# Kernel tuning notes

Measured on AMD Instinct MI355X. Metric: run time of the kernel, lower is better.

Reference implementation:

```python
import jax, jax.numpy as jnp
import numpy as np

EMBED_DIM = 256
NUM_HEADS = 8
WINDOW = 64
HEAD_DIM = EMBED_DIM // NUM_HEADS


def setup_inputs() -> dict:
    key = jax.random.key(0)
    k_x, k_w, k_ow = jax.random.split(key, 3)
    B, S, E = 2, 4096, EMBED_DIM
    x = jax.random.normal(k_x, (B, S, E), dtype=jnp.float32)
    # nn.MultiheadAttention params: packed in_proj (q,k,v) and out_proj
    bound = 1.0 / np.sqrt(E)
    in_proj_w = jax.random.uniform(k_w, (3 * E, E), jnp.float32, -bound, bound)
    in_proj_b = jnp.zeros((3 * E,), jnp.float32)
    out_w = jax.random.uniform(k_ow, (E, E), jnp.float32, -bound, bound)
    out_b = jnp.zeros((E,), jnp.float32)
    return {"x": x, "in_proj_w": in_proj_w, "in_proj_b": in_proj_b,
            "out_w": out_w, "out_b": out_b}


def reference(x, in_proj_w, in_proj_b, out_w, out_b):
    B, S, E = x.shape
    H, D = NUM_HEADS, HEAD_DIM
    # packed qkv projection (torch Linear: y = x @ W^T + b)
    qkv = jnp.einsum('bse,fe->bsf', x, in_proj_w) + in_proj_b  # [B,S,3E]
    q, k, v = jnp.split(qkv, 3, axis=-1)
    q = q.reshape(B, S, H, D).transpose(0, 2, 1, 3)  # [B,H,S,D]
    k = k.reshape(B, S, H, D).transpose(0, 2, 1, 3)
    v = v.reshape(B, S, H, D).transpose(0, 2, 1, 3)
    scale = 1.0 / jnp.sqrt(jnp.asarray(D, x.dtype))
    scores = jnp.einsum('bhqd,bhkd->bhqk', q * scale, k)  # [B,H,S,S]
    idx = jnp.arange(S)
    band = jnp.abs(idx[:, None] - idx[None, :]) <= WINDOW  # [S,S]
    neg = jnp.asarray(-1e9, scores.dtype)
    scores = jnp.where(band[None, None, :, :], scores, neg)
    attn = jax.nn.softmax(scores, axis=-1)
    out = jnp.einsum('bhqk,bhkd->bhqd', attn, v)  # [B,H,S,D]
    out = out.transpose(0, 2, 1, 3).reshape(B, S, E)
    return jnp.einsum('bse,fe->bsf', out, out_w) + out_b
```

## Files before the change

### kernel.cpp

```cpp
#include <hip/hip_runtime.h>
#include <hip/hip_bf16.h>

#define S_LEN 4096
#define EMB   256
#define NHEAD 8
#define HDIM  32
#define WIN   64
#define BATCH 2

typedef __attribute__((ext_vector_type(8))) short short8;
typedef __attribute__((ext_vector_type(4))) float floatx4;
typedef unsigned short u16;
typedef unsigned int   u32;

static __device__ __forceinline__ u32 bf16_rn(float x) {
    u32 u = __float_as_uint(x);
    return (u + 0x7FFFu + ((u >> 16) & 1u)) >> 16;
}
static __device__ __forceinline__ u32 packsplit(float x) {
    const u32 hi = bf16_rn(x);
    const float hf = __uint_as_float(hi << 16);
    const u32 lo = bf16_rn(x - hf);
    return (hi << 16) | lo;
}
static __device__ __forceinline__ void unpack_pair(u32 p0, u32 p1, u32& h, u32& l) {
    h = (p0 >> 16) | (p1 & 0xFFFF0000u);
    l = (p0 & 0xFFFFu) | (p1 << 16);
}
static __device__ __forceinline__ void unpack8(uint4 a, uint4 b, uint4& h, uint4& l) {
    unpack_pair(a.x, a.y, h.x, l.x);
    unpack_pair(a.z, a.w, h.y, l.y);
    unpack_pair(b.x, b.y, h.z, l.z);
    unpack_pair(b.z, b.w, h.w, l.w);
}

#define NX4 524288
#define NW4 49152
#define NO4 16384

__global__ __launch_bounds__(256) void convert_kernel(
    const float* __restrict__ X, const float* __restrict__ Wi, const float* __restrict__ Wo,
    u32* __restrict__ Xp, u32* __restrict__ Wip, u32* __restrict__ Wop)
{
    const int i = blockIdx.x * 256 + threadIdx.x;
    const float* src; u32* dst; int off;
    if (i < NX4)            { src = X;  dst = Xp;  off = i; }
    else if (i < NX4 + NW4) { src = Wi; dst = Wip; off = i - NX4; }
    else                    { src = Wo; dst = Wop; off = i - NX4 - NW4; }
    const float4 v = *(const float4*)(src + (size_t)off * 4);
    uint4 o;
    o.x = packsplit(v.x); o.y = packsplit(v.y);
    o.z = packsplit(v.z); o.w = packsplit(v.w);
    *(uint4*)(dst + (size_t)off * 4) = o;
}

#define LDA 40

__global__ __launch_bounds__(256) void qkv_proj_kernel(
    const u32* __restrict__ Xp, const u32* __restrict__ Wp,
    const float* __restrict__ bias,
    u32* __restrict__ Qp, u32* __restrict__ Kp, u32* __restrict__ Vp)
{
    __shared__ __align__(16) u16 Ah[128 * LDA], Al[128 * LDA];
    __shared__ __align__(16) u16 Bh[64 * LDA],  Bl[64 * LDA];
    const int tid = threadIdx.x;
    const int m0 = blockIdx.y * 128, n0 = blockIdx.x * 64;
    const int srow = tid >> 2, sc = tid & 3;
    const int lane = tid & 63, wv = tid >> 6;
    const int wm = (wv >> 1) * 64, wn = (wv & 1) * 32;
    const int lm = lane & 15, kq = lane >> 4;

    uint4 pA[2][2], pB[2];
#pragma unroll
    for (int r = 0; r < 2; ++r) {
        const u32* base = Xp + (size_t)(m0 + srow + r * 64) * EMB + sc * 8;
        pA[r][0] = *(const uint4*)base;
        pA[r][1] = *(const uint4*)(base + 4);
    }
    {
        const u32* base = Wp + (size_t)(n0 + srow) * EMB + sc * 8;
        pB[0] = *(const uint4*)base;
        pB[1] = *(const uint4*)(base + 4);
    }

    floatx4 acc[4][2] = {};
    for (int t = 0; t < 8; ++t) {
        __syncthreads();
#pragma unroll
        for (int r = 0; r < 2; ++r) {
            uint4 h, l;
            unpack8(pA[r][0], pA[r][1], h, l);
            *(uint4*)&Ah[(srow + r * 64) * LDA + sc * 8] = h;
            *(uint4*)&Al[(srow + r * 64) * LDA + sc * 8] = l;
        }
        {
            uint4 h, l;
            unpack8(pB[0], pB[1], h, l);
            *(uint4*)&Bh[srow * LDA + sc * 8] = h;
            *(uint4*)&Bl[srow * LDA + sc * 8] = l;
        }
        __syncthreads();
        if (t < 7) {
            const int k0 = (t + 1) * 32;
#pragma unroll
            for (int r = 0; r < 2; ++r) {
                const u32* base = Xp + (size_t)(m0 + srow + r * 64) * EMB + k0 + sc * 8;
                pA[r][0] = *(const uint4*)base;
                pA[r][1] = *(const uint4*)(base + 4);
            }
            const u32* base = Wp + (size_t)(n0 + srow) * EMB + k0 + sc * 8;
            pB[0] = *(const uint4*)base;
            pB[1] = *(const uint4*)(base + 4);
        }
        short8 a_h[4], a_l[4], b_h[2], b_l[2];
#pragma unroll
        for (int mt = 0; mt < 4; ++mt) {
            a_h[mt] = *(const short8*)&Ah[(wm + mt * 16 + lm) * LDA + kq * 8];
            a_l[mt] = *(const short8*)&Al[(wm + mt * 16 + lm) * LDA + kq * 8];
        }
#pragma unroll
        for (int nt = 0; nt < 2; ++nt) {
            b_h[nt] = *(const short8*)&Bh[(wn + nt * 16 + lm) * LDA + kq * 8];
            b_l[nt] = *(const short8*)&Bl[(wn + nt * 16 + lm) * LDA + kq * 8];
        }
#pragma unroll
        for (int mt = 0; mt < 4; ++mt)
#pragma unroll
            for (int nt = 0; nt < 2; ++nt) {
                acc[mt][nt] = __builtin_amdgcn_mfma_f32_16x16x32_bf16(a_h[mt], b_h[nt], acc[mt][nt], 0, 0, 0);
                acc[mt][nt] = __builtin_amdgcn_mfma_f32_16x16x32_bf16(a_h[mt], b_l[nt], acc[mt][nt], 0, 0, 0);
                acc[mt][nt] = __builtin_amdgcn_mfma_f32_16x16x32_bf16(a_l[mt], b_h[nt], acc[mt][nt], 0, 0, 0);
            }
    }
#pragma unroll
    for (int nt = 0; nt < 2; ++nt) {
        const int f = n0 + wn + nt * 16 + lm;
        const int which = f >> 8;
        const int h = (f & 255) >> 5, d = f & 31;
        u32* dst = (which == 0) ? Qp : ((which == 1) ? Kp : Vp);
        const float sc2 = (which == 0) ? 0.17677669529663687f : 1.0f;
        const float bf = bias[f];
#pragma unroll
        for (int mt = 0; mt < 4; ++mt)
#pragma unroll
            for (int r = 0; r < 4; ++r) {
                const int m = m0 + wm + mt * 16 + kq * 4 + r;
                const int b = m >> 12, s = m & (S_LEN - 1);
                dst[(((size_t)b * NHEAD + h) * S_LEN + s) * HDIM + d]
                    = packsplit((acc[mt][nt][r] + bf) * sc2);
            }
    }
}

__global__ __launch_bounds__(256) void out_proj_kernel(
    const u32* __restrict__ Abp, const u32* __restrict__ Wp,
    const float* __restrict__ bias, float* __restrict__ C)
{
    __shared__ __align__(16) u16 Ah[64 * LDA], Al[64 * LDA];
    __shared__ __align__(16) u16 Bh[64 * LDA], Bl[64 * LDA];
    const int tid = threadIdx.x;
    const int m0 = blockIdx.y * 64, n0 = blockIdx.x * 64;
    const int srow = tid >> 2, sc = tid & 3;
    const int lane = tid & 63, wv = tid >> 6;
    const int wm = (wv >> 1) * 32, wn = (wv & 1) * 32;
    const int lm = lane & 15, kq = lane >> 4;

    uint4 pA[2], pB[2];
    {
        const u32* base = Abp + (size_t)(m0 + srow) * EMB + sc * 8;
        pA[0] = *(const uint4*)base;
        pA[1] = *(const uint4*)(base + 4);
    }
    {
        const u32* base = Wp + (size_t)(n0 + srow) * EMB + sc * 8;
        pB[0] = *(const uint4*)base;
        pB[1] = *(const uint4*)(base + 4);
    }

    floatx4 acc[2][2] = {};
    for (int t = 0; t < 8; ++t) {
        __syncthreads();
        {
            uint4 h, l;
            unpack8(pA[0], pA[1], h, l);
            *(uint4*)&Ah[srow * LDA + sc * 8] = h;
            *(uint4*)&Al[srow * LDA + sc * 8] = l;
        }
        {
            uint4 h, l;
            unpack8(pB[0], pB[1], h, l);
            *(uint4*)&Bh[srow * LDA + sc * 8] = h;
            *(uint4*)&Bl[srow * LDA + sc * 8] = l;
        }
        __syncthreads();
        if (t < 7) {
            const int k0 = (t + 1) * 32;
            {
                const u32* base = Abp + (size_t)(m0 + srow) * EMB + k0 + sc * 8;
                pA[0] = *(const uint4*)base;
                pA[1] = *(const uint4*)(base + 4);
            }
            const u32* base = Wp + (size_t)(n0 + srow) * EMB + k0 + sc * 8;
            pB[0] = *(const uint4*)base;
            pB[1] = *(const uint4*)(base + 4);
        }
        short8 a_h[2], a_l[2], b_h[2], b_l[2];
#pragma unroll
        for (int mt = 0; mt < 2; ++mt) {
            a_h[mt] = *(const short8*)&Ah[(wm + mt * 16 + lm) * LDA + kq * 8];
            a_l[mt] = *(const short8*)&Al[(wm + mt * 16 + lm) * LDA + kq * 8];
        }
#pragma unroll
        for (int nt = 0; nt < 2; ++nt) {
            b_h[nt] = *(const short8*)&Bh[(wn + nt * 16 + lm) * LDA + kq * 8];
            b_l[nt] = *(const short8*)&Bl[(wn + nt * 16 + lm) * LDA + kq * 8];
        }
#pragma unroll
        for (int mt = 0; mt < 2; ++mt)
#pragma unroll
            for (int nt = 0; nt < 2; ++nt) {
                acc[mt][nt] = __builtin_amdgcn_mfma_f32_16x16x32_bf16(a_h[mt], b_h[nt], acc[mt][nt], 0, 0, 0);
                acc[mt][nt] = __builtin_amdgcn_mfma_f32_16x16x32_bf16(a_h[mt], b_l[nt], acc[mt][nt], 0, 0, 0);
                acc[mt][nt] = __builtin_amdgcn_mfma_f32_16x16x32_bf16(a_l[mt], b_h[nt], acc[mt][nt], 0, 0, 0);
            }
    }
#pragma unroll
    for (int nt = 0; nt < 2; ++nt) {
        const int f = n0 + wn + nt * 16 + lm;
        const float bf = bias[f];
#pragma unroll
        for (int mt = 0; mt < 2; ++mt)
#pragma unroll
            for (int r = 0; r < 4; ++r) {
                const int m = m0 + wm + mt * 16 + kq * 4 + r;
                C[(size_t)m * EMB + f] = acc[mt][nt][r] + bf;
            }
    }
}

#define AKS 40
#define AVS 200

__global__ __launch_bounds__(256) void local_attn_kernel(
    const u32* __restrict__ Qp, const u32* __restrict__ Kp,
    const u32* __restrict__ Vp, u32* __restrict__ Abp)
{
    __shared__ __align__(16) u16 Kh[192 * AKS], Kl[192 * AKS];
    __shared__ __align__(16) u16 Vt[32 * AVS];

    const int tid = threadIdx.x;
    const int q0 = blockIdx.x * 64;
    const int h = blockIdx.y, b = blockIdx.z;
    const int jmin = max(0, q0 - WIN);
    const int jmax = min(S_LEN - 1, q0 + 63 + WIN);
    const int nk = jmax - jmin + 1;
    const size_t bhS = ((size_t)b * NHEAD + h) * S_LEN;
    const size_t qoff = (bhS + q0) * HDIM;
    const size_t koff = (bhS + jmin) * HDIM;

    const int lane = tid & 63, wv = tid >> 6;
    const int lm = lane & 15, quad = lane >> 4;
    const int qbase = wv * 16;

    const u32* qb = Qp + qoff + (size_t)(qbase + lm) * HDIM + quad * 8;
    const uint4 qp0 = *(const uint4*)qb;
    const uint4 qp1 = *(const uint4*)(qb + 4);

    const int srow = tid >> 2, sc = tid & 3;
#pragma unroll
    for (int r = 0; r < 3; ++r) {
        const int t = srow + r * 64;
        const int tc = min(t, nk - 1);
        const u32* base = Kp + koff + (size_t)tc * HDIM + sc * 8;
        uint4 h4, l4;
        unpack8(*(const uint4*)base, *(const uint4*)(base + 4), h4, l4);
        *(uint4*)&Kh[t * AKS + sc * 8] = h4;
        *(uint4*)&Kl[t * AKS + sc * 8] = l4;
    }
#pragma unroll
    for (int r = 0; r < 3; ++r) {
        const int t = srow + r * 64;
        const int tc = min(t, nk - 1);
        const u32* base = Vp + koff + (size_t)tc * HDIM + sc * 8;
        const uint4 v0 = *(const uint4*)base;
        const uint4 v1 = *(const uint4*)(base + 4);
        const int d0 = sc * 8;
        Vt[(d0 + 0) * AVS + t] = (u16)(v0.x >> 16);
        Vt[(d0 + 1) * AVS + t] = (u16)(v0.y >> 16);
        Vt[(d0 + 2) * AVS + t] = (u16)(v0.z >> 16);
        Vt[(d0 + 3) * AVS + t] = (u16)(v0.w >> 16);
        Vt[(d0 + 4) * AVS + t] = (u16)(v1.x >> 16);
        Vt[(d0 + 5) * AVS + t] = (u16)(v1.y >> 16);
        Vt[(d0 + 6) * AVS + t] = (u16)(v1.z >> 16);
        Vt[(d0 + 7) * AVS + t] = (u16)(v1.w >> 16);
    }

    short8 qh, ql;
    {
        uint4 h4, l4;
        unpack8(qp0, qp1, h4, l4);
        qh = *(const short8*)&h4;
        ql = *(const short8*)&l4;
    }

    __syncthreads();

    const int tb = max(0, ((wv >> 1) << 1) + (min(q0 - WIN, 0) >> 4));

    floatx4 sacc[10];
#pragma unroll
    for (int i = 0; i < 10; ++i) {
        const int nt = tb + i;
        const short8 kh = *(const short8*)&Kh[(nt * 16 + lm) * AKS + quad * 8];
        const short8 kl = *(const short8*)&Kl[(nt * 16 + lm) * AKS + quad * 8];
        floatx4 a = {};
        a = __builtin_amdgcn_mfma_f32_16x16x32_bf16(kh, qh, a, 0, 0, 0);
        a = __builtin_amdgcn_mfma_f32_16x16x32_bf16(kh, ql, a, 0, 0, 0);
        a = __builtin_amdgcn_mfma_f32_16x16x32_bf16(kl, qh, a, 0, 0, 0);
        sacc[i] = a;
    }

    const int qr = q0 + qbase + lm;
    float mx = -1e30f;
#pragma unroll
    for (int i = 0; i < 10; ++i) {
        const int sbase = (tb + i) * 16 + quad * 4;
#pragma unroll
        for (int r = 0; r < 4; ++r) {
            const int slot = sbase + r;
            const int keyg = jmin + slot;
            const bool valid = (slot < nk) && (keyg >= qr - WIN) && (keyg <= qr + WIN);
            const float sv = valid ? sacc[i][r] : -1e30f;
            sacc[i][r] = sv;
            mx = fmaxf(mx, sv);
        }
    }
    mx = fmaxf(mx, __shfl_xor(mx, 16));
    mx = fmaxf(mx, __shfl_xor(mx, 32));

    float l = 0.f;
    u32 pk_[20];
#pragma unroll
    for (int i = 0; i < 10; ++i) {
        const float p0 = __expf(sacc[i][0] - mx);
        const float p1 = __expf(sacc[i][1] - mx);
        const float p2 = __expf(sacc[i][2] - mx);
        const float p3 = __expf(sacc[i][3] - mx);
        l += (p0 + p1) + (p2 + p3);
        pk_[2 * i]     = bf16_rn(p0) | (bf16_rn(p1) << 16);
        pk_[2 * i + 1] = bf16_rn(p2) | (bf16_rn(p3) << 16);
    }
    l += __shfl_xor(l, 16);
    l += __shfl_xor(l, 32);
    const float rl = 1.f / l;

    const int kb = tb >> 1;
    floatx4 oacc[2] = {};
#pragma unroll
    for (int i = 0; i < 5; ++i) {
        const int ks = kb + i;
        uint4 aw;
        aw.x = pk_[4 * i + 0];
        aw.y = pk_[4 * i + 1];
        aw.z = pk_[4 * i + 2];
        aw.w = pk_[4 * i + 3];
        const short8 ap = *(const short8*)&aw;
        const int sb = ks * 32 + quad * 4;
        const uint2 e0 = *(const uint2*)&Vt[lm * AVS + sb];
        const uint2 o0 = *(const uint2*)&Vt[lm * AVS + sb + 16];
        const uint2 e1 = *(const uint2*)&Vt[(16 + lm) * AVS + sb];
        const uint2 o1 = *(const uint2*)&Vt[(16 + lm) * AVS + sb + 16];
        uint4 bw0; bw0.x = e0.x; bw0.y = e0.y; bw0.z = o0.x; bw0.w = o0.y;
        uint4 bw1; bw1.x = e1.x; bw1.y = e1.y; bw1.z = o1.x; bw1.w = o1.y;
        const short8 bv0 = *(const short8*)&bw0;
        const short8 bv1 = *(const short8*)&bw1;
        oacc[0] = __builtin_amdgcn_mfma_f32_16x16x32_bf16(ap, bv0, oacc[0], 0, 0, 0);
        oacc[1] = __builtin_amdgcn_mfma_f32_16x16x32_bf16(ap, bv1, oacc[1], 0, 0, 0);
    }

    float rlr[4];
#pragma unroll
    for (int r = 0; r < 4; ++r) rlr[r] = __shfl(rl, quad * 4 + r);
#pragma unroll
    for (int nt = 0; nt < 2; ++nt)
#pragma unroll
        for (int r = 0; r < 4; ++r) {
            const int qrow = qbase + quad * 4 + r;
            Abp[((size_t)b * S_LEN + q0 + qrow) * EMB + h * HDIM + nt * 16 + lm]
                = packsplit(oacc[nt][r] * rlr[r]);
        }
}

extern "C" void kernel_launch(void* const* d_in, const int* in_sizes, int n_in,
                              void* d_out, int out_size, void* d_ws, size_t ws_size,
                              hipStream_t stream) {
    const float* x  = (const float*)d_in[0];
    const float* wi = (const float*)d_in[1];
    const float* bi = (const float*)d_in[2];
    const float* wo = (const float*)d_in[3];
    const float* bo = (const float*)d_in[4];
    float* out = (float*)d_out;

    const size_t per = (size_t)BATCH * NHEAD * S_LEN * HDIM;
    u32* p = (u32*)d_ws;
    u32* Xp  = p; p += per;
    u32* Wip = p; p += 768 * EMB;
    u32* Wop = p; p += EMB * EMB;
    u32* Qp  = p; p += per;
    u32* Kp  = p; p += per;
    u32* Vp  = p; p += per;
    u32* Abp = p; p += per;

    convert_kernel<<<dim3((NX4 + NW4 + NO4) / 256), 256, 0, stream>>>(
        x, wi, wo, Xp, Wip, Wop);
    qkv_proj_kernel<<<dim3(768 / 64, 8192 / 128), 256, 0, stream>>>(
        Xp, Wip, bi, Qp, Kp, Vp);
    local_attn_kernel<<<dim3(S_LEN / 64, NHEAD, BATCH), 256, 0, stream>>>(
        Qp, Kp, Vp, Abp);
    out_proj_kernel<<<dim3(256 / 64, 8192 / 64), 256, 0, stream>>>(
        Abp, Wop, bo, out);
}
```

Baseline: 110.9 us.

## Split hi/lo bf16 planes and stage GEMM tiles via direct global-to-LDS loads

Intermediate tensors are stored as separate hi and lo bf16 planes instead of interleaved packed u32, which removes the unpack shuffles in every consumer. V now keeps only its hi plane, since only that part was ever used. The projection GEMMs load tiles with global_load_lds into double-buffered, XOR-swizzled LDS, and remap the block order for locality. This gives up register prefetching and padded LDS for a direct async copy path with one barrier per k-step. That path depends on swizzle correctness and on whether the hardware honours the 16-byte LDS load.

```diff
diff --git a/kernel.cpp b/kernel.cpp
--- a/kernel.cpp
+++ b/kernel.cpp
@@ -10,6 +10,7 @@
 
 typedef __attribute__((ext_vector_type(8))) short short8;
 typedef __attribute__((ext_vector_type(4))) float floatx4;
+typedef __attribute__((ext_vector_type(4))) unsigned short ushort4v;
 typedef unsigned short u16;
 typedef unsigned int   u32;
 
@@ -17,21 +18,11 @@
     u32 u = __float_as_uint(x);
     return (u + 0x7FFFu + ((u >> 16) & 1u)) >> 16;
 }
-static __device__ __forceinline__ u32 packsplit(float x) {
-    const u32 hi = bf16_rn(x);
-    const float hf = __uint_as_float(hi << 16);
-    const u32 lo = bf16_rn(x - hf);
-    return (hi << 16) | lo;
-}
-static __device__ __forceinline__ void unpack_pair(u32 p0, u32 p1, u32& h, u32& l) {
-    h = (p0 >> 16) | (p1 & 0xFFFF0000u);
-    l = (p0 & 0xFFFFu) | (p1 << 16);
-}
-static __device__ __forceinline__ void unpack8(uint4 a, uint4 b, uint4& h, uint4& l) {
-    unpack_pair(a.x, a.y, h.x, l.x);
-    unpack_pair(a.z, a.w, h.y, l.y);
-    unpack_pair(b.x, b.y, h.z, l.z);
-    unpack_pair(b.z, b.w, h.w, l.w);
+
+static __device__ __forceinline__ void gload16(const u16* g, u16* l) {
+    __builtin_amdgcn_global_load_lds(
+        (const __attribute__((address_space(1))) void*)g,
+        (__attribute__((address_space(3))) void*)l, 16, 0, 0);
 }
 
 #define NX4 524288
@@ -40,88 +31,83 @@
 
 __global__ __launch_bounds__(256) void convert_kernel(
     const float* __restrict__ X, const float* __restrict__ Wi, const float* __restrict__ Wo,
-    u32* __restrict__ Xp, u32* __restrict__ Wip, u32* __restrict__ Wop)
+    u16* __restrict__ Xh, u16* __restrict__ Xl,
+    u16* __restrict__ Wih, u16* __restrict__ Wil,
+    u16* __restrict__ Woh, u16* __restrict__ Wol)
 {
     const int i = blockIdx.x * 256 + threadIdx.x;
-    const float* src; u32* dst; int off;
-    if (i < NX4)            { src = X;  dst = Xp;  off = i; }
-    else if (i < NX4 + NW4) { src = Wi; dst = Wip; off = i - NX4; }
-    else                    { src = Wo; dst = Wop; off = i - NX4 - NW4; }
+    const float* src; u16 *dh, *dl; int off;
+    if (i < NX4)            { src = X;  dh = Xh;  dl = Xl;  off = i; }
+    else if (i < NX4 + NW4) { src = Wi; dh = Wih; dl = Wil; off = i - NX4; }
+    else                    { src = Wo; dh = Woh; dl = Wol; off = i - NX4 - NW4; }
     const float4 v = *(const float4*)(src + (size_t)off * 4);
-    uint4 o;
-    o.x = packsplit(v.x); o.y = packsplit(v.y);
-    o.z = packsplit(v.z); o.w = packsplit(v.w);
-    *(uint4*)(dst + (size_t)off * 4) = o;
-}
-
-#define LDA 40
+    ushort4v h, l;
+    {
+        u32 hb;
+        hb = bf16_rn(v.x); h.x = (u16)hb; l.x = (u16)bf16_rn(v.x - __uint_as_float(hb << 16));
+        hb = bf16_rn(v.y); h.y = (u16)hb; l.y = (u16)bf16_rn(v.y - __uint_as_float(hb << 16));
+        hb = bf16_rn(v.z); h.z = (u16)hb; l.z = (u16)bf16_rn(v.z - __uint_as_float(hb << 16));
+        hb = bf16_rn(v.w); h.w = (u16)hb; l.w = (u16)bf16_rn(v.w - __uint_as_float(hb << 16));
+    }
+    *(ushort4v*)(dh + (size_t)off * 4) = h;
+    *(ushort4v*)(dl + (size_t)off * 4) = l;
+}
+
+#define BK 32
 
 __global__ __launch_bounds__(256) void qkv_proj_kernel(
-    const u32* __restrict__ Xp, const u32* __restrict__ Wp,
+    const u16* __restrict__ Xh, const u16* __restrict__ Xl,
+    const u16* __restrict__ Wh, const u16* __restrict__ Wl,
     const float* __restrict__ bias,
-    u32* __restrict__ Qp, u32* __restrict__ Kp, u32* __restrict__ Vp)
+    u16* __restrict__ Qh, u16* __restrict__ Ql,
+    u16* __restrict__ Kh, u16* __restrict__ Kl,
+    u16* __restrict__ Vh)
 {
-    __shared__ __align__(16) u16 Ah[128 * LDA], Al[128 * LDA];
-    __shared__ __align__(16) u16 Bh[64 * LDA],  Bl[64 * LDA];
+    __shared__ __align__(16) u16 SA[2][2][128 * BK];
+    __shared__ __align__(16) u16 SB[2][2][64 * BK];
+
     const int tid = threadIdx.x;
-    const int m0 = blockIdx.y * 128, n0 = blockIdx.x * 64;
-    const int srow = tid >> 2, sc = tid & 3;
+    const int wg0 = blockIdx.y * 12 + blockIdx.x;
+    const int wg = (wg0 & 7) * 96 + (wg0 >> 3);
+    const int n0 = (wg % 12) * 64, m0 = (wg / 12) * 128;
     const int lane = tid & 63, wv = tid >> 6;
+    const int lm = lane & 15, kq = lane >> 4;
+    const int gr = lane >> 2;
+    const int gc = ((lane & 3) ^ ((lane >> 3) & 3)) * 8;
+    const int swz = (lm >> 1) & 3;
     const int wm = (wv >> 1) * 64, wn = (wv & 1) * 32;
-    const int lm = lane & 15, kq = lane >> 4;
-
-    uint4 pA[2][2], pB[2];
-#pragma unroll
-    for (int r = 0; r < 2; ++r) {
-        const u32* base = Xp + (size_t)(m0 + srow + r * 64) * EMB + sc * 8;
-        pA[r][0] = *(const uint4*)base;
-        pA[r][1] = *(const uint4*)(base + 4);
-    }
-    {
-        const u32* base = Wp + (size_t)(n0 + srow) * EMB + sc * 8;
-        pB[0] = *(const uint4*)base;
-        pB[1] = *(const uint4*)(base + 4);
-    }
+
+    auto stage = [&](int buf, int k0) {
+#pragma unroll
+        for (int cc = 0; cc < 2; ++cc) {
+            const int c = 2 * wv + cc;
+            const size_t grow = (size_t)(m0 + 16 * c + gr) * EMB + k0 + gc;
+            gload16(Xh + grow, &SA[buf][0][c * 512]);
+            gload16(Xl + grow, &SA[buf][1][c * 512]);
+        }
+        const size_t brow = (size_t)(n0 + 16 * wv + gr) * EMB + k0 + gc;
+        gload16(Wh + brow, &SB[buf][0][wv * 512]);
+        gload16(Wl + brow, &SB[buf][1][wv * 512]);
+    };
 
     floatx4 acc[4][2] = {};
+    stage(0, 0);
+    __syncthreads();
+    int cur = 0;
     for (int t = 0; t < 8; ++t) {
-        __syncthreads();
-#pragma unroll
-        for (int r = 0; r < 2; ++r) {
-            uint4 h, l;
-            unpack8(pA[r][0], pA[r][1], h, l);
-            *(uint4*)&Ah[(srow + r * 64) * LDA + sc * 8] = h;
-            *(uint4*)&Al[(srow + r * 64) * LDA + sc * 8] = l;
-        }
-        {
-            uint4 h, l;
-            unpack8(pB[0], pB[1], h, l);
-            *(uint4*)&Bh[srow * LDA + sc * 8] = h;
-            *(uint4*)&Bl[srow * LDA + sc * 8] = l;
-        }
-        __syncthreads();
-        if (t < 7) {
-            const int k0 = (t + 1) * 32;
-#pragma unroll
-            for (int r = 0; r < 2; ++r) {
-                const u32* base = Xp + (size_t)(m0 + srow + r * 64) * EMB + k0 + sc * 8;
-                pA[r][0] = *(const uint4*)base;
-                pA[r][1] = *(const uint4*)(base + 4);
-            }
-            const u32* base = Wp + (size_t)(n0 + srow) * EMB + k0 + sc * 8;
-            pB[0] = *(const uint4*)base;
-            pB[1] = *(const uint4*)(base + 4);
-        }
+        if (t < 7) stage(cur ^ 1, (t + 1) * 32);
         short8 a_h[4], a_l[4], b_h[2], b_l[2];
 #pragma unroll
         for (int mt = 0; mt < 4; ++mt) {
-            a_h[mt] = *(const short8*)&Ah[(wm + mt * 16 + lm) * LDA + kq * 8];
-            a_l[mt] = *(const short8*)&Al[(wm + mt * 16 + lm) * LDA + kq * 8];
+            const int ro = (wm + mt * 16 + lm) * BK + (kq ^ swz) * 8;
+            a_h[mt] = *(const short8*)&SA[cur][0][ro];
+            a_l[mt] = *(const short8*)&SA[cur][1][ro];
         }
 #pragma unroll
         for (int nt = 0; nt < 2; ++nt) {
-            b_h[nt] = *(const short8*)&Bh[(wn + nt * 16 + lm) * LDA + kq * 8];
-            b_l[nt] = *(const short8*)&Bl[(wn + nt * 16 + lm) * LDA + kq * 8];
+            const int ro = (wn + nt * 16 + lm) * BK + (kq ^ swz) * 8;
+            b_h[nt] = *(const short8*)&SB[cur][0][ro];
+            b_l[nt] = *(const short8*)&SB[cur][1][ro];
         }
 #pragma unroll
         for (int mt = 0; mt < 4; ++mt)
@@ -131,13 +117,16 @@
                 acc[mt][nt] = __builtin_amdgcn_mfma_f32_16x16x32_bf16(a_h[mt], b_l[nt], acc[mt][nt], 0, 0, 0);
                 acc[mt][nt] = __builtin_amdgcn_mfma_f32_16x16x32_bf16(a_l[mt], b_h[nt], acc[mt][nt], 0, 0, 0);
             }
+        __syncthreads();
+        cur ^= 1;
     }
 #pragma unroll
     for (int nt = 0; nt < 2; ++nt) {
         const int f = n0 + wn + nt * 16 + lm;
         const int which = f >> 8;
-        const int h = (f & 255) >> 5, d = f & 31;
-        u32* dst = (which == 0) ? Qp : ((which == 1) ? Kp : Vp);
+        const int hh = (f & 255) >> 5, d = f & 31;
+        u16* dh = (which == 0) ? Qh : ((which == 1) ? Kh : Vh);
+        u16* dl = (which == 0) ? Ql : Kl;
         const float sc2 = (which == 0) ? 0.17677669529663687f : 1.0f;
         const float bf = bias[f];
 #pragma unroll
@@ -146,74 +135,61 @@
             for (int r = 0; r < 4; ++r) {
                 const int m = m0 + wm + mt * 16 + kq * 4 + r;
                 const int b = m >> 12, s = m & (S_LEN - 1);
-                dst[(((size_t)b * NHEAD + h) * S_LEN + s) * HDIM + d]
-                    = packsplit((acc[mt][nt][r] + bf) * sc2);
+                const size_t idx = (((size_t)b * NHEAD + hh) * S_LEN + s) * HDIM + d;
+                const float val = (acc[mt][nt][r] + bf) * sc2;
+                const u32 hbits = bf16_rn(val);
+                dh[idx] = (u16)hbits;
+                if (which != 2)
+                    dl[idx] = (u16)bf16_rn(val - __uint_as_float(hbits << 16));
             }
     }
 }
 
 __global__ __launch_bounds__(256) void out_proj_kernel(
-    const u32* __restrict__ Abp, const u32* __restrict__ Wp,
+    const u16* __restrict__ Ahp, const u16* __restrict__ Alp,
+    const u16* __restrict__ Wh, const u16* __restrict__ Wl,
     const float* __restrict__ bias, float* __restrict__ C)
 {
-    __shared__ __align__(16) u16 Ah[64 * LDA], Al[64 * LDA];
-    __shared__ __align__(16) u16 Bh[64 * LDA], Bl[64 * LDA];
+    __shared__ __align__(16) u16 SA[2][2][64 * BK];
+    __shared__ __align__(16) u16 SB[2][2][64 * BK];
     const int tid = threadIdx.x;
-    const int m0 = blockIdx.y * 64, n0 = blockIdx.x * 64;
-    const int srow = tid >> 2, sc = tid & 3;
+    const int wg0 = blockIdx.y * 4 + blockIdx.x;
+    const int wg = (wg0 & 7) * 64 + (wg0 >> 3);
+    const int n0 = (wg & 3) * 64, m0 = (wg >> 2) * 64;
     const int lane = tid & 63, wv = tid >> 6;
+    const int lm = lane & 15, kq = lane >> 4;
+    const int gr = lane >> 2;
+    const int gc = ((lane & 3) ^ ((lane >> 3) & 3)) * 8;
+    const int swz = (lm >> 1) & 3;
     const int wm = (wv >> 1) * 32, wn = (wv & 1) * 32;
-    const int lm = lane & 15, kq = lane >> 4;
-
-    uint4 pA[2], pB[2];
-    {
-        const u32* base = Abp + (size_t)(m0 + srow) * EMB + sc * 8;
-        pA[0] = *(const uint4*)base;
-        pA[1] = *(const uint4*)(base + 4);
-    }
-    {
-        const u32* base = Wp + (size_t)(n0 + srow) * EMB + sc * 8;
-        pB[0] = *(const uint4*)base;
-        pB[1] = *(const uint4*)(base + 4);
-    }
+
+    auto stage = [&](int buf, int k0) {
+        const size_t arow = (size_t)(m0 + 16 * wv + gr) * EMB + k0 + gc;
+        gload16(Ahp + arow, &SA[buf][0][wv * 512]);
+        gload16(Alp + arow, &SA[buf][1][wv * 512]);
+        const size_t brow = (size_t)(n0 + 16 * wv + gr) * EMB + k0 + gc;
+        gload16(Wh + brow, &SB[buf][0][wv * 512]);
+        gload16(Wl + brow, &SB[buf][1][wv * 512]);
+    };
 
     floatx4 acc[2][2] = {};
+    stage(0, 0);
+    __syncthreads();
+    int cur = 0;
     for (int t = 0; t < 8; ++t) {
-        __syncthreads();
-        {
-            uint4 h, l;
-            unpack8(pA[0], pA[1], h, l);
-            *(uint4*)&Ah[srow * LDA + sc * 8] = h;
-            *(uint4*)&Al[srow * LDA + sc * 8] = l;
-        }
-        {
-            uint4 h, l;
-            unpack8(pB[0], pB[1], h, l);
-            *(uint4*)&Bh[srow * LDA + sc * 8] = h;
-            *(uint4*)&Bl[srow * LDA + sc * 8] = l;
-        }
-        __syncthreads();
-        if (t < 7) {
-            const int k0 = (t + 1) * 32;
-            {
-                const u32* base = Abp + (size_t)(m0 + srow) * EMB + k0 + sc * 8;
-                pA[0] = *(const uint4*)base;
-                pA[1] = *(const uint4*)(base + 4);
-            }
-            const u32* base = Wp + (size_t)(n0 + srow) * EMB + k0 + sc * 8;
-            pB[0] = *(const uint4*)base;
-            pB[1] = *(const uint4*)(base + 4);
-        }
+        if (t < 7) stage(cur ^ 1, (t + 1) * 32);
         short8 a_h[2], a_l[2], b_h[2], b_l[2];
 #pragma unroll
         for (int mt = 0; mt < 2; ++mt) {
-            a_h[mt] = *(const short8*)&Ah[(wm + mt * 16 + lm) * LDA + kq * 8];
-            a_l[mt] = *(const short8*)&Al[(wm + mt * 16 + lm) * LDA + kq * 8];
+            const int ro = (wm + mt * 16 + lm) * BK + (kq ^ swz) * 8;
+            a_h[mt] = *(const short8*)&SA[cur][0][ro];
+            a_l[mt] = *(const short8*)&SA[cur][1][ro];
         }
 #pragma unroll
         for (int nt = 0; nt < 2; ++nt) {
-            b_h[nt] = *(const short8*)&Bh[(wn + nt * 16 + lm) * LDA + kq * 8];
-            b_l[nt] = *(const short8*)&Bl[(wn + nt * 16 + lm) * LDA + kq * 8];
+            const int ro = (wn + nt * 16 + lm) * BK + (kq ^ swz) * 8;
+            b_h[nt] = *(const short8*)&SB[cur][0][ro];
+            b_l[nt] = *(const short8*)&SB[cur][1][ro];
         }
 #pragma unroll
         for (int mt = 0; mt < 2; ++mt)
@@ -223,6 +199,8 @@
                 acc[mt][nt] = __builtin_amdgcn_mfma_f32_16x16x32_bf16(a_h[mt], b_l[nt], acc[mt][nt], 0, 0, 0);
                 acc[mt][nt] = __builtin_amdgcn_mfma_f32_16x16x32_bf16(a_l[mt], b_h[nt], acc[mt][nt], 0, 0, 0);
             }
+        __syncthreads();
+        cur ^= 1;
     }
 #pragma unroll
     for (int nt = 0; nt < 2; ++nt) {
@@ -242,11 +220,13 @@
 #define AVS 200
 
 __global__ __launch_bounds__(256) void local_attn_kernel(
-    const u32* __restrict__ Qp, const u32* __restrict__ Kp,
-    const u32* __restrict__ Vp, u32* __restrict__ Abp)
+    const u16* __restrict__ Qhg, const u16* __restrict__ Qlg,
+    const u16* __restrict__ Khg, const u16* __restrict__ Klg,
+    const u16* __restrict__ Vhg,
+    u16* __restrict__ Abh, u16* __restrict__ Abl)
 {
-    __shared__ __align__(16) u16 Kh[192 * AKS], Kl[192 * AKS];
-    __shared__ __align__(16) u16 Vt[32 * AVS];
+    __shared__ __align__(16) u16 sKh[192 * AKS], sKl[192 * AKS];
+    __shared__ __align__(16) u16 sVt[32 * AVS];
 
     const int tid = threadIdx.x;
     const int q0 = blockIdx.x * 64;
@@ -262,47 +242,28 @@
     const int lm = lane & 15, quad = lane >> 4;
     const int qbase = wv * 16;
 
-    const u32* qb = Qp + qoff + (size_t)(qbase + lm) * HDIM + quad * 8;
-    const uint4 qp0 = *(const uint4*)qb;
-    const uint4 qp1 = *(const uint4*)(qb + 4);
+    const short8 qh = *(const short8*)(Qhg + qoff + (size_t)(qbase + lm) * HDIM + quad * 8);
+    const short8 ql = *(const short8*)(Qlg + qoff + (size_t)(qbase + lm) * HDIM + quad * 8);
 
     const int srow = tid >> 2, sc = tid & 3;
 #pragma unroll
     for (int r = 0; r < 3; ++r) {
         const int t = srow + r * 64;
         const int tc = min(t, nk - 1);
-        const u32* base = Kp + koff + (size_t)tc * HDIM + sc * 8;
-        uint4 h4, l4;
-        unpack8(*(const uint4*)base, *(const uint4*)(base + 4), h4, l4);
-        *(uint4*)&Kh[t * AKS + sc * 8] = h4;
-        *(uint4*)&Kl[t * AKS + sc * 8] = l4;
+        const size_t go = koff + (size_t)tc * HDIM + sc * 8;
+        *(short8*)&sKh[t * AKS + sc * 8] = *(const short8*)(Khg + go);
+        *(short8*)&sKl[t * AKS + sc * 8] = *(const short8*)(Klg + go);
     }
 #pragma unroll
     for (int r = 0; r < 3; ++r) {
         const int t = srow + r * 64;
         const int tc = min(t, nk - 1);
-        const u32* base = Vp + koff + (size_t)tc * HDIM + sc * 8;
-        const uint4 v0 = *(const uint4*)base;
-        const uint4 v1 = *(const uint4*)(base + 4);
+        const short8 v = *(const short8*)(Vhg + koff + (size_t)tc * HDIM + sc * 8);
         const int d0 = sc * 8;
-        Vt[(d0 + 0) * AVS + t] = (u16)(v0.x >> 16);
-        Vt[(d0 + 1) * AVS + t] = (u16)(v0.y >> 16);
-        Vt[(d0 + 2) * AVS + t] = (u16)(v0.z >> 16);
-        Vt[(d0 + 3) * AVS + t] = (u16)(v0.w >> 16);
-        Vt[(d0 + 4) * AVS + t] = (u16)(v1.x >> 16);
-        Vt[(d0 + 5) * AVS + t] = (u16)(v1.y >> 16);
-        Vt[(d0 + 6) * AVS + t] = (u16)(v1.z >> 16);
-        Vt[(d0 + 7) * AVS + t] = (u16)(v1.w >> 16);
-    }
-
-    short8 qh, ql;
-    {
-        uint4 h4, l4;
-        unpack8(qp0, qp1, h4, l4);
-        qh = *(const short8*)&h4;
-        ql = *(const short8*)&l4;
-    }
-
+#pragma unroll
+        for (int j = 0; j < 8; ++j)
+            sVt[(d0 + j) * AVS + t] = (u16)v[j];
+    }
     __syncthreads();
 
     const int tb = max(0, ((wv >> 1) << 1) + (min(q0 - WIN, 0) >> 4));
@@ -311,8 +272,8 @@
 #pragma unroll
     for (int i = 0; i < 10; ++i) {
         const int nt = tb + i;
-        const short8 kh = *(const short8*)&Kh[(nt * 16 + lm) * AKS + quad * 8];
-        const short8 kl = *(const short8*)&Kl[(nt * 16 + lm) * AKS + quad * 8];
+        const short8 kh = *(const short8*)&sKh[(nt * 16 + lm) * AKS + quad * 8];
+        const short8 kl = *(const short8*)&sKl[(nt * 16 + lm) * AKS + quad * 8];
         floatx4 a = {};
         a = __builtin_amdgcn_mfma_f32_16x16x32_bf16(kh, qh, a, 0, 0, 0);
         a = __builtin_amdgcn_mfma_f32_16x16x32_bf16(kh, ql, a, 0, 0, 0);
@@ -366,10 +327,10 @@
         aw.w = pk_[4 * i + 3];
         const short8 ap = *(const short8*)&aw;
         const int sb = ks * 32 + quad * 4;
-        const uint2 e0 = *(const uint2*)&Vt[lm * AVS + sb];
-        const uint2 o0 = *(const uint2*)&Vt[lm * AVS + sb + 16];
-        const uint2 e1 = *(const uint2*)&Vt[(16 + lm) * AVS + sb];
-        const uint2 o1 = *(const uint2*)&Vt[(16 + lm) * AVS + sb + 16];
+        const uint2 e0 = *(const uint2*)&sVt[lm * AVS + sb];
+        const uint2 o0 = *(const uint2*)&sVt[lm * AVS + sb + 16];
+        const uint2 e1 = *(const uint2*)&sVt[(16 + lm) * AVS + sb];
+        const uint2 o1 = *(const uint2*)&sVt[(16 + lm) * AVS + sb + 16];
         uint4 bw0; bw0.x = e0.x; bw0.y = e0.y; bw0.z = o0.x; bw0.w = o0.y;
         uint4 bw1; bw1.x = e1.x; bw1.y = e1.y; bw1.z = o1.x; bw1.w = o1.y;
         const short8 bv0 = *(const short8*)&bw0;
@@ -386,8 +347,11 @@
 #pragma unroll
         for (int r = 0; r < 4; ++r) {
             const int qrow = qbase + quad * 4 + r;
-            Abp[((size_t)b * S_LEN + q0 + qrow) * EMB + h * HDIM + nt * 16 + lm]
-                = packsplit(oacc[nt][r] * rlr[r]);
+            const float o = oacc[nt][r] * rlr[r];
+            const u32 hb = bf16_rn(o);
+            const size_t idx = ((size_t)b * S_LEN + q0 + qrow) * EMB + h * HDIM + nt * 16 + lm;
+            Abh[idx] = (u16)hb;
+            Abl[idx] = (u16)bf16_rn(o - __uint_as_float(hb << 16));
         }
 }
 
@@ -402,21 +366,27 @@
     float* out = (float*)d_out;
 
     const size_t per = (size_t)BATCH * NHEAD * S_LEN * HDIM;
-    u32* p = (u32*)d_ws;
-    u32* Xp  = p; p += per;
-    u32* Wip = p; p += 768 * EMB;
-    u32* Wop = p; p += EMB * EMB;
-    u32* Qp  = p; p += per;
-    u32* Kp  = p; p += per;
-    u32* Vp  = p; p += per;
-    u32* Abp = p; p += per;
+    u16* p = (u16*)d_ws;
+    u16* Xh  = p; p += per;
+    u16* Xl  = p; p += per;
+    u16* Wih = p; p += 768 * EMB;
+    u16* Wil = p; p += 768 * EMB;
+    u16* Woh = p; p += EMB * EMB;
+    u16* Wol = p; p += EMB * EMB;
+    u16* Qh  = p; p += per;
+    u16* Ql  = p; p += per;
+    u16* Kh  = p; p += per;
+    u16* Kl  = p; p += per;
+    u16* Vh  = p; p += per;
+    u16* Abh = p; p += per;
+    u16* Abl = p; p += per;
 
     convert_kernel<<<dim3((NX4 + NW4 + NO4) / 256), 256, 0, stream>>>(
-        x, wi, wo, Xp, Wip, Wop);
+        x, wi, wo, Xh, Xl, Wih, Wil, Woh, Wol);
     qkv_proj_kernel<<<dim3(768 / 64, 8192 / 128), 256, 0, stream>>>(
-        Xp, Wip, bi, Qp, Kp, Vp);
+        Xh, Xl, Wih, Wil, bi, Qh, Ql, Kh, Kl, Vh);
     local_attn_kernel<<<dim3(S_LEN / 64, NHEAD, BATCH), 256, 0, stream>>>(
-        Qp, Kp, Vp, Abp);
+        Qh, Ql, Kh, Kl, Vh, Abh, Abl);
     out_proj_kernel<<<dim3(256 / 64, 8192 / 64), 256, 0, stream>>>(
-        Abp, Wop, bo, out);
-}
+        Abh, Abl, Woh, Wol, bo, out);
+}
```

Measured after the change: 108.2 us. 1.02x faster.
